# Performance work log

Hardware: AMD Instinct MI355X
Metric: run time of the kernel (lower is better)

Reference implementation:

```python
import jax, jax.numpy as jnp
import numpy as np

B, S, HID = 1, 2048, 1024
NH, NKV, HD = 16, 4, 64
SCALING = 0.125  # attention_multiplier = 1/sqrt(head_dim)
ROPE_THETA = 10000.0
NEG_MIN = jnp.finfo(jnp.float32).min


def rotate_half(x):
    x1, x2 = jnp.split(x, 2, axis=-1)
    return jnp.concatenate([-x2, x1], axis=-1)


def setup_inputs() -> dict:
    key = jax.random.key(0)
    ks = jax.random.split(key, 6)
    hidden_states = jax.random.normal(ks[0], (B, S, HID), dtype=jnp.float32)
    # RoPE tables: [1, 1, S, HD]
    inv_freq = 1.0 / (ROPE_THETA ** (np.arange(0, HD, 2, dtype=np.float32) / HD))
    t = np.arange(S, dtype=np.float32)
    freqs = np.outer(t, inv_freq)                      # [S, HD/2]
    emb = np.concatenate([freqs, freqs], axis=-1)      # [S, HD]
    cos = jnp.asarray(np.cos(emb))[None, None]
    sin = jnp.asarray(np.sin(emb))[None, None]
    attention_mask = jnp.ones((B, S), dtype=bool)
    sc = 0.02
    Wq = jax.random.normal(ks[1], (HID, NH * HD), dtype=jnp.float32) * sc
    Wk = jax.random.normal(ks[2], (HID, NKV * HD), dtype=jnp.float32) * sc
    Wv = jax.random.normal(ks[3], (HID, NKV * HD), dtype=jnp.float32) * sc
    Wo = jax.random.normal(ks[4], (NH * HD, HID), dtype=jnp.float32) * sc
    return {"hidden_states": hidden_states, "cos": cos, "sin": sin,
            "attention_mask": attention_mask, "Wq": Wq, "Wk": Wk, "Wv": Wv, "Wo": Wo}


def reference(hidden_states, cos, sin, attention_mask, Wq, Wk, Wv, Wo):
    b, s, _ = hidden_states.shape
    # projections -> [B, H, S, D]
    q = (hidden_states @ Wq).reshape(b, s, NH, HD).transpose(0, 2, 1, 3)
    k = (hidden_states @ Wk).reshape(b, s, NKV, HD).transpose(0, 2, 1, 3)
    v = (hidden_states @ Wv).reshape(b, s, NKV, HD).transpose(0, 2, 1, 3)
    # RoPE (full head_dim rotation; cos/sin broadcast over batch/heads)
    q = q * cos + rotate_half(q) * sin
    k = k * cos + rotate_half(k) * sin
    # repeat_kv: expand kv heads to match query heads
    n_rep = NH // NKV
    k = jnp.repeat(k, n_rep, axis=1)
    v = jnp.repeat(v, n_rep, axis=1)
    # scores: [B, H, Sq, Sk]
    attn = jnp.einsum('bhqd,bhkd->bhqk', q, k) * SCALING
    mask = attention_mask[:, None, None, :].astype(attn.dtype)  # bool padding mask
    attn = attn + (1.0 - mask) * NEG_MIN
    attn = jax.nn.softmax(attn.astype(jnp.float32), axis=-1).astype(q.dtype)
    out = jnp.einsum('bhqk,bhkd->bhqd', attn, v)
    out = out.transpose(0, 2, 1, 3).reshape(b, s, NH * HD)
    return out @ Wo
```

## Files before the change

kernel.cpp:

```cpp
#include <hip/hip_runtime.h>
#include <stdint.h>

typedef __attribute__((ext_vector_type(8))) short short8;
typedef __attribute__((ext_vector_type(4))) short short4v;
typedef __attribute__((ext_vector_type(4))) float floatx4;
typedef __attribute__((ext_vector_type(16))) float floatx16;
typedef __attribute__((ext_vector_type(2))) unsigned int uint2v;
typedef __attribute__((ext_vector_type(4))) unsigned int uint4v;

#define AS1 __attribute__((address_space(1)))
#define AS3 __attribute__((address_space(3)))

__device__ __forceinline__ void async16(const void* g, void* l) {
  __builtin_amdgcn_global_load_lds((const AS1 unsigned int*)g, (AS3 unsigned int*)l, 16, 0, 0);
}

__device__ __forceinline__ short f2bf(float f) {
  unsigned u = __float_as_uint(f);
  u = (u + 0x7FFF + ((u >> 16) & 1)) >> 16;
  return (short)u;
}

#if __has_builtin(__builtin_amdgcn_cvt_pk_bf16_f32)
typedef __bf16 bf16x2 __attribute__((ext_vector_type(2)));
__device__ __forceinline__ unsigned pack2(float lo, float hi) {
  bf16x2 t = __builtin_amdgcn_cvt_pk_bf16_f32(lo, hi);
  return *(unsigned*)&t;
}
#else
__device__ __forceinline__ unsigned pack2(float lo, float hi) {
  return __builtin_amdgcn_perm(__float_as_uint(hi) + 0x8000u,
                               __float_as_uint(lo) + 0x8000u, 0x07060302u);
}
#endif

__device__ __forceinline__ uint2v permswap32(unsigned a, unsigned b) {
#if __has_builtin(__builtin_amdgcn_permlane32_swap)
  return __builtin_amdgcn_permlane32_swap(a, b, false, false);
#else
  asm volatile("v_permlane32_swap_b32 %0, %1" : "+v"(a), "+v"(b));
  uint2v r; r.x = a; r.y = b; return r;
#endif
}

__device__ __forceinline__ void stage_sw(const short* src, int stride,
                                         short* tile, int cb, int lane) {
  int i = cb + lane;
  int r = i >> 3, j = i & 7;
  async16(src + (size_t)r * stride + ((j ^ (r & 7)) * 8), tile + cb * 8);
}
__device__ __forceinline__ int sw(int row, int c8) {
  return row * 64 + ((c8 ^ (row & 7)) * 8);
}

__global__ void k_prep(const float* __restrict__ X, const float* __restrict__ Wq,
                       const float* __restrict__ Wk, const float* __restrict__ Wv,
                       const float* __restrict__ Wo, short* __restrict__ Xb,
                       short* __restrict__ Wqkvt, short* __restrict__ Wot) {
  int b = blockIdx.x, tid = threadIdx.x;
  if (b < 2048) {
    int i = b * 1024 + tid * 4;
    floatx4 v = *(const floatx4*)(X + i);
    short4v o;
    o.x = f2bf(v.x); o.y = f2bf(v.y); o.z = f2bf(v.z); o.w = f2bf(v.w);
    *(short4v*)(Xb + i) = o;
    return;
  }
  const float* src; short* dst; int N, brel, rowoff;
  if (b < 3072)      { src = Wq; dst = Wqkvt; N = 1024; brel = b - 2048; rowoff = 0; }
  else if (b < 3328) { src = Wk; dst = Wqkvt; N = 256;  brel = b - 3072; rowoff = 1024; }
  else if (b < 3584) { src = Wv; dst = Wqkvt; N = 256;  brel = b - 3328; rowoff = 1280; }
  else               { src = Wo; dst = Wot;   N = 1024; brel = b - 3584; rowoff = 0; }
  __shared__ short t[32][33];
  int nt = N >> 5;
  int n0 = (brel % nt) * 32, k0 = (brel / nt) * 32;
  int tx = tid & 31, ty = tid >> 5;
#pragma unroll
  for (int i = 0; i < 4; i++)
    t[ty + 8 * i][tx] = f2bf(src[(size_t)(k0 + ty + 8 * i) * N + n0 + tx]);
  __syncthreads();
#pragma unroll
  for (int i = 0; i < 4; i++)
    dst[(size_t)(rowoff + n0 + ty + 8 * i) * 1024 + k0 + tx] = t[tx][ty + 8 * i];
}

__global__ __launch_bounds__(256) void k_gemmqkv(const short* __restrict__ A,
                                                 const short* __restrict__ Bt,
                                                 short* __restrict__ Qb,
                                                 short* __restrict__ Kb,
                                                 short* __restrict__ Vtb,
                                                 const float* __restrict__ cosp,
                                                 const float* __restrict__ sinp,
                                                 float qscale) {
  int tid = threadIdx.x;
  int flat = blockIdx.y * 24 + blockIdx.x;
  int swz = (flat & 7) * 96 + (flat >> 3);
  int bx = swz % 24, by = swz / 24;
  int w = tid >> 6, lane = tid & 63, quad = lane >> 4, l16 = lane & 15;
  __shared__ short As[2][4096];
  __shared__ short Bs[2][4096];
  const int K = 1024;
  const short* Ag = A + (size_t)(by * 64) * K;
  const short* Bg = Bt + (size_t)(bx * 64) * K;
  floatx4 acc[4] = {};
#pragma unroll
  for (int t = 0; t < 2; t++) stage_sw(Ag, K, As[0], (w * 2 + t) * 64, lane);
#pragma unroll
  for (int t = 0; t < 2; t++) stage_sw(Bg, K, Bs[0], (w * 2 + t) * 64, lane);
  for (int kt = 0; kt < 16; kt++) {
    __syncthreads();
    int cur = kt & 1, nxt = cur ^ 1;
    if (kt + 1 < 16) {
#pragma unroll
      for (int t = 0; t < 2; t++) stage_sw(Ag + (kt + 1) * 64, K, As[nxt], (w * 2 + t) * 64, lane);
#pragma unroll
      for (int t = 0; t < 2; t++) stage_sw(Bg + (kt + 1) * 64, K, Bs[nxt], (w * 2 + t) * 64, lane);
    }
#pragma unroll
    for (int ks = 0; ks < 2; ks++) {
      short8 af = *(const short8*)&As[cur][sw(w * 16 + l16, ks * 4 + quad)];
#pragma unroll
      for (int j = 0; j < 4; j++) {
        short8 bfr = *(const short8*)&Bs[cur][sw(j * 16 + l16, ks * 4 + quad)];
        acc[j] = __builtin_amdgcn_mfma_f32_16x16x32_bf16(af, bfr, acc[j], 0, 0, 0);
      }
    }
  }
  if (bx < 20) {
    short* dst; float scale;
    if (bx < 16) { dst = Qb + (size_t)bx * 2048 * 64; scale = qscale; }
    else         { dst = Kb + (size_t)(bx - 16) * 2048 * 64; scale = 1.0f; }
#pragma unroll
    for (int r = 0; r < 4; r++) {
      int s = by * 64 + w * 16 + quad * 4 + r;
#pragma unroll
      for (int j = 0; j < 2; j++) {
        int d = j * 16 + l16;
        float c = cosp[s * 64 + d], sn = sinp[s * 64 + d];
        float v0 = acc[j][r], v1 = acc[j + 2][r];
        dst[(size_t)s * 64 + d]      = f2bf((v0 * c - v1 * sn) * scale);
        dst[(size_t)s * 64 + 32 + d] = f2bf((v1 * c + v0 * sn) * scale);
      }
    }
  } else {
    short* dst = Vtb + (size_t)(bx - 20) * 64 * 2048;
#pragma unroll
    for (int j = 0; j < 4; j++) {
      int d = j * 16 + l16;
      short4v pk;
#pragma unroll
      for (int r = 0; r < 4; r++) pk[r] = f2bf(acc[j][r]);
      *(short4v*)&dst[(size_t)d * 2048 + by * 64 + w * 16 + quad * 4] = pk;
    }
  }
}

__global__ __launch_bounds__(256) void k_gemm(const short* __restrict__ A,
                                              const short* __restrict__ Bt,
                                              float* __restrict__ C,
                                              int M, int N, int K) {
  int tid = threadIdx.x;
  int flat = blockIdx.y * 16 + blockIdx.x;
  int swz = (flat & 7) * 64 + (flat >> 3);
  int bx = swz & 15, by = swz >> 4;
  int w = tid >> 6, lane = tid & 63, quad = lane >> 4, l16 = lane & 15;
  __shared__ short As[2][4096];
  __shared__ short Bs[2][4096];
  const short* Ag = A + (size_t)(by * 64) * K;
  const short* Bg = Bt + (size_t)(bx * 64) * K;
  floatx4 acc[4] = {};
  int kiters = K >> 6;
#pragma unroll
  for (int t = 0; t < 2; t++) stage_sw(Ag, K, As[0], (w * 2 + t) * 64, lane);
#pragma unroll
  for (int t = 0; t < 2; t++) stage_sw(Bg, K, Bs[0], (w * 2 + t) * 64, lane);
  for (int kt = 0; kt < kiters; kt++) {
    __syncthreads();
    int cur = kt & 1, nxt = cur ^ 1;
    if (kt + 1 < kiters) {
#pragma unroll
      for (int t = 0; t < 2; t++) stage_sw(Ag + (kt + 1) * 64, K, As[nxt], (w * 2 + t) * 64, lane);
#pragma unroll
      for (int t = 0; t < 2; t++) stage_sw(Bg + (kt + 1) * 64, K, Bs[nxt], (w * 2 + t) * 64, lane);
    }
#pragma unroll
    for (int ks = 0; ks < 2; ks++) {
      short8 af = *(const short8*)&As[cur][sw(w * 16 + l16, ks * 4 + quad)];
#pragma unroll
      for (int j = 0; j < 4; j++) {
        short8 bfr = *(const short8*)&Bs[cur][sw(j * 16 + l16, ks * 4 + quad)];
        acc[j] = __builtin_amdgcn_mfma_f32_16x16x32_bf16(af, bfr, acc[j], 0, 0, 0);
      }
    }
  }
#pragma unroll
  for (int j = 0; j < 4; j++)
#pragma unroll
    for (int r = 0; r < 4; r++) {
      int row = by * 64 + w * 16 + quad * 4 + r;
      int col = bx * 64 + j * 16 + l16;
      __builtin_nontemporal_store(acc[j][r], &C[(size_t)row * N + col]);
    }
}

__global__ __launch_bounds__(256, 4) void k_attn(const short* __restrict__ Qb,
                                                 const short* __restrict__ Kb,
                                                 const short* __restrict__ Vt,
                                                 float* __restrict__ Opart,
                                                 float* __restrict__ lpart) {
  int flat = (blockIdx.z * 16 + blockIdx.y) * 16 + blockIdx.x;
  int swz = (flat & 7) * 128 + (flat >> 3);
  int qt = swz & 15;
  int h = (swz >> 4) & 15;
  int sp = swz >> 8;
  int kvh = h >> 2;
  int tid = threadIdx.x, w = tid >> 6, lane = tid & 63;
  int l32 = lane & 31, hi = lane >> 5;
  __shared__ short Ks[2][4096];
  __shared__ short Vs[2][4096];
  const short* Qg = Qb + ((size_t)h * 2048 + qt * 128 + w * 32) * 64;
  const short* Kg0 = Kb + ((size_t)kvh * 2048 + sp * 512) * 64;
  const short* Vg0 = Vt + (size_t)kvh * 64 * 2048 + sp * 512;
  short8 qf[4];
#pragma unroll
  for (int ks4 = 0; ks4 < 4; ks4++)
    qf[ks4] = *(const short8*)(Qg + l32 * 64 + ks4 * 16 + hi * 8);
#pragma unroll
  for (int t = 0; t < 2; t++) stage_sw(Kg0, 64, Ks[0], (w * 2 + t) * 64, lane);
#pragma unroll
  for (int t = 0; t < 2; t++) stage_sw(Vg0, 2048, Vs[0], (w * 2 + t) * 64, lane);
  short8 vones;
  {
    short one = (short)0x3F80;
#pragma unroll
    for (int j = 0; j < 8; j++) vones[j] = (l32 == 0) ? one : (short)0;
  }
  floatx16 accO[2] = {};
  floatx16 accL = {};
  for (int kt = 0; kt < 8; kt++) {
    __syncthreads();
    if (kt + 1 < 8) {
      int nb = (kt + 1) & 1;
#pragma unroll
      for (int t = 0; t < 2; t++)
        stage_sw(Kg0 + (kt + 1) * 4096, 64, Ks[nb], (w * 2 + t) * 64, lane);
#pragma unroll
      for (int t = 0; t < 2; t++)
        stage_sw(Vg0 + (kt + 1) * 64, 2048, Vs[nb], (w * 2 + t) * 64, lane);
    }
    int cu = kt & 1;
#pragma unroll
    for (int kb = 0; kb < 2; kb++) {
      floatx16 accS = {};
#pragma unroll
      for (int ks4 = 0; ks4 < 4; ks4++) {
        short8 af = *(const short8*)&Ks[cu][sw(kb * 32 + l32, ks4 * 2 + hi)];
        accS = __builtin_amdgcn_mfma_f32_32x32x16_bf16(af, qf[ks4], accS, 0, 0, 0);
      }
#pragma unroll
      for (int c = 0; c < 2; c++) {
        float p0 = __builtin_amdgcn_exp2f(accS[8 * c + 0]);
        float p1 = __builtin_amdgcn_exp2f(accS[8 * c + 1]);
        float p2 = __builtin_amdgcn_exp2f(accS[8 * c + 2]);
        float p3 = __builtin_amdgcn_exp2f(accS[8 * c + 3]);
        float p4 = __builtin_amdgcn_exp2f(accS[8 * c + 4]);
        float p5 = __builtin_amdgcn_exp2f(accS[8 * c + 5]);
        float p6 = __builtin_amdgcn_exp2f(accS[8 * c + 6]);
        float p7 = __builtin_amdgcn_exp2f(accS[8 * c + 7]);
        uint2v r0 = permswap32(pack2(p0, p1), pack2(p4, p5));
        uint2v r1 = permswap32(pack2(p2, p3), pack2(p6, p7));
        uint4v pw; pw.x = r0.x; pw.y = r1.x; pw.z = r0.y; pw.w = r1.y;
        short8 pa = *(short8*)&pw;
        int kstep = kb * 2 + c;
        accL = __builtin_amdgcn_mfma_f32_32x32x16_bf16(pa, vones, accL, 0, 0, 0);
#pragma unroll
        for (int db = 0; db < 2; db++) {
          short8 vf = *(const short8*)&Vs[cu][sw(db * 32 + l32, kstep * 2 + hi)];
          accO[db] = __builtin_amdgcn_mfma_f32_32x32x16_bf16(pa, vf, accO[db], 0, 0, 0);
        }
      }
    }
  }
  if (l32 == 0) {
#pragma unroll
    for (int reg = 0; reg < 16; reg++) {
      int q = (reg & 3) + 8 * (reg >> 2) + 4 * hi;
      __builtin_nontemporal_store(accL[reg],
          &lpart[(size_t)sp * 16 * 2048 + h * 2048 + qt * 128 + w * 32 + q]);
    }
  }
  float* Op = Opart + (size_t)sp * 2048 * 1024;
#pragma unroll
  for (int db = 0; db < 2; db++)
#pragma unroll
    for (int reg = 0; reg < 16; reg++) {
      int q = (reg & 3) + 8 * (reg >> 2) + 4 * hi;
      int srow = qt * 128 + w * 32 + q;
      int col = h * 64 + db * 32 + l32;
      __builtin_nontemporal_store(accO[db][reg], &Op[(size_t)srow * 1024 + col]);
    }
}

__global__ void k_comb(const float* __restrict__ Opart, const float* __restrict__ lpart,
                       short* __restrict__ AOb) {
  int idx = (blockIdx.x * 256 + threadIdx.x) * 4;
  int s = idx >> 10, h = (idx & 1023) >> 6;
  float l = 0.f;
#pragma unroll
  for (int sp = 0; sp < 4; sp++)
    l += __builtin_nontemporal_load(&lpart[sp * 16 * 2048 + h * 2048 + s]);
  float inv = 1.0f / l;
  floatx4 a = __builtin_nontemporal_load((const floatx4*)(Opart + idx));
#pragma unroll
  for (int sp = 1; sp < 4; sp++) {
    floatx4 b = __builtin_nontemporal_load(
        (const floatx4*)(Opart + (size_t)sp * 2048 * 1024 + idx));
    a.x += b.x; a.y += b.y; a.z += b.z; a.w += b.w;
  }
  uint2v pk;
  pk.x = pack2(a.x * inv, a.y * inv);
  pk.y = pack2(a.z * inv, a.w * inv);
  *(uint2v*)&AOb[idx] = pk;
}

extern "C" void kernel_launch(void* const* d_in, const int* in_sizes, int n_in,
                              void* d_out, int out_size, void* d_ws, size_t ws_size,
                              hipStream_t stream) {
  const float* X    = (const float*)d_in[0];
  const float* cosp = (const float*)d_in[1];
  const float* sinp = (const float*)d_in[2];
  const float* Wq = (const float*)d_in[4];
  const float* Wk = (const float*)d_in[5];
  const float* Wv = (const float*)d_in[6];
  const float* Wo = (const float*)d_in[7];
  float* out = (float*)d_out;

  short* Xb    = (short*)d_ws;
  short* Wqkvt = Xb + 2097152;
  short* Wot   = Wqkvt + 1572864;
  short* Qb2   = Wot + 1048576;
  short* Kb2   = Qb2 + 2097152;
  short* Vtb   = Kb2 + 524288;
  short* AOb   = Vtb + 524288;
  float* Opart = (float*)(AOb + 2097152);
  float* lpart = Opart + 4 * 2097152;

  const float QSCALE = 0.125f * 1.44269504088896340736f;

  k_prep<<<4608, 256, 0, stream>>>(X, Wq, Wk, Wv, Wo, Xb, Wqkvt, Wot);
  k_gemmqkv<<<dim3(24, 32), 256, 0, stream>>>(Xb, Wqkvt, Qb2, Kb2, Vtb, cosp, sinp, QSCALE);
  k_attn<<<dim3(16, 16, 4), 256, 0, stream>>>(Qb2, Kb2, Vtb, Opart, lpart);
  k_comb<<<2048, 256, 0, stream>>>(Opart, lpart, AOb);
  k_gemm<<<dim3(16, 32), 256, 0, stream>>>(AOb, Wot, out, 2048, 1024, 1024);
}
```

Before: 138.3 us.

## Process two query groups per wave in attention to reuse K/V fragments

The attention kernel now runs 2 waves per block instead of 4, and each wave handles 64 query rows as two 32-row groups. K and V fragments are loaded from LDS once per key block and reused across both groups, halving LDS reads per MFMA. Each wave also issues twice the staging copies. The cost is more accumulator registers per wave and fewer waves per block, which may lower occupancy and latency hiding.

```diff
diff --git a/kernel.cpp b/kernel.cpp
--- a/kernel.cpp
+++ b/kernel.cpp
@@ -203,7 +203,7 @@
     }
 }
 
-__global__ __launch_bounds__(256, 4) void k_attn(const short* __restrict__ Qb,
+__global__ __launch_bounds__(128, 2) void k_attn(const short* __restrict__ Qb,
                                                  const short* __restrict__ Kb,
                                                  const short* __restrict__ Vt,
                                                  float* __restrict__ Opart,
@@ -218,87 +218,101 @@
   int l32 = lane & 31, hi = lane >> 5;
   __shared__ short Ks[2][4096];
   __shared__ short Vs[2][4096];
-  const short* Qg = Qb + ((size_t)h * 2048 + qt * 128 + w * 32) * 64;
+  const short* Qg = Qb + ((size_t)h * 2048 + qt * 128 + w * 64) * 64;
   const short* Kg0 = Kb + ((size_t)kvh * 2048 + sp * 512) * 64;
   const short* Vg0 = Vt + (size_t)kvh * 64 * 2048 + sp * 512;
-  short8 qf[4];
-#pragma unroll
-  for (int ks4 = 0; ks4 < 4; ks4++)
-    qf[ks4] = *(const short8*)(Qg + l32 * 64 + ks4 * 16 + hi * 8);
-#pragma unroll
-  for (int t = 0; t < 2; t++) stage_sw(Kg0, 64, Ks[0], (w * 2 + t) * 64, lane);
-#pragma unroll
-  for (int t = 0; t < 2; t++) stage_sw(Vg0, 2048, Vs[0], (w * 2 + t) * 64, lane);
+  short8 qf[2][4];
+#pragma unroll
+  for (int g = 0; g < 2; g++)
+#pragma unroll
+    for (int ks4 = 0; ks4 < 4; ks4++)
+      qf[g][ks4] = *(const short8*)(Qg + (g * 32 + l32) * 64 + ks4 * 16 + hi * 8);
+#pragma unroll
+  for (int t = 0; t < 4; t++) stage_sw(Kg0, 64, Ks[0], (w * 4 + t) * 64, lane);
+#pragma unroll
+  for (int t = 0; t < 4; t++) stage_sw(Vg0, 2048, Vs[0], (w * 4 + t) * 64, lane);
   short8 vones;
   {
     short one = (short)0x3F80;
 #pragma unroll
     for (int j = 0; j < 8; j++) vones[j] = (l32 == 0) ? one : (short)0;
   }
-  floatx16 accO[2] = {};
-  floatx16 accL = {};
+  floatx16 accO[2][2] = {};
+  floatx16 accL[2] = {};
   for (int kt = 0; kt < 8; kt++) {
     __syncthreads();
     if (kt + 1 < 8) {
       int nb = (kt + 1) & 1;
 #pragma unroll
-      for (int t = 0; t < 2; t++)
-        stage_sw(Kg0 + (kt + 1) * 4096, 64, Ks[nb], (w * 2 + t) * 64, lane);
-#pragma unroll
-      for (int t = 0; t < 2; t++)
-        stage_sw(Vg0 + (kt + 1) * 64, 2048, Vs[nb], (w * 2 + t) * 64, lane);
+      for (int t = 0; t < 4; t++)
+        stage_sw(Kg0 + (kt + 1) * 4096, 64, Ks[nb], (w * 4 + t) * 64, lane);
+#pragma unroll
+      for (int t = 0; t < 4; t++)
+        stage_sw(Vg0 + (kt + 1) * 64, 2048, Vs[nb], (w * 4 + t) * 64, lane);
     }
     int cu = kt & 1;
 #pragma unroll
     for (int kb = 0; kb < 2; kb++) {
-      floatx16 accS = {};
-#pragma unroll
-      for (int ks4 = 0; ks4 < 4; ks4++) {
-        short8 af = *(const short8*)&Ks[cu][sw(kb * 32 + l32, ks4 * 2 + hi)];
-        accS = __builtin_amdgcn_mfma_f32_32x32x16_bf16(af, qf[ks4], accS, 0, 0, 0);
-      }
-#pragma unroll
-      for (int c = 0; c < 2; c++) {
-        float p0 = __builtin_amdgcn_exp2f(accS[8 * c + 0]);
-        float p1 = __builtin_amdgcn_exp2f(accS[8 * c + 1]);
-        float p2 = __builtin_amdgcn_exp2f(accS[8 * c + 2]);
-        float p3 = __builtin_amdgcn_exp2f(accS[8 * c + 3]);
-        float p4 = __builtin_amdgcn_exp2f(accS[8 * c + 4]);
-        float p5 = __builtin_amdgcn_exp2f(accS[8 * c + 5]);
-        float p6 = __builtin_amdgcn_exp2f(accS[8 * c + 6]);
-        float p7 = __builtin_amdgcn_exp2f(accS[8 * c + 7]);
-        uint2v r0 = permswap32(pack2(p0, p1), pack2(p4, p5));
-        uint2v r1 = permswap32(pack2(p2, p3), pack2(p6, p7));
-        uint4v pw; pw.x = r0.x; pw.y = r1.x; pw.z = r0.y; pw.w = r1.y;
-        short8 pa = *(short8*)&pw;
-        int kstep = kb * 2 + c;
-        accL = __builtin_amdgcn_mfma_f32_32x32x16_bf16(pa, vones, accL, 0, 0, 0);
-#pragma unroll
-        for (int db = 0; db < 2; db++) {
-          short8 vf = *(const short8*)&Vs[cu][sw(db * 32 + l32, kstep * 2 + hi)];
-          accO[db] = __builtin_amdgcn_mfma_f32_32x32x16_bf16(pa, vf, accO[db], 0, 0, 0);
+      short8 af[4];
+#pragma unroll
+      for (int ks4 = 0; ks4 < 4; ks4++)
+        af[ks4] = *(const short8*)&Ks[cu][sw(kb * 32 + l32, ks4 * 2 + hi)];
+      short8 vf[2][2];
+#pragma unroll
+      for (int c = 0; c < 2; c++)
+#pragma unroll
+        for (int db = 0; db < 2; db++)
+          vf[c][db] = *(const short8*)&Vs[cu][sw(db * 32 + l32, (kb * 2 + c) * 2 + hi)];
+#pragma unroll
+      for (int g = 0; g < 2; g++) {
+        floatx16 accS = {};
+#pragma unroll
+        for (int ks4 = 0; ks4 < 4; ks4++)
+          accS = __builtin_amdgcn_mfma_f32_32x32x16_bf16(af[ks4], qf[g][ks4], accS, 0, 0, 0);
+#pragma unroll
+        for (int c = 0; c < 2; c++) {
+          float p0 = __builtin_amdgcn_exp2f(accS[8 * c + 0]);
+          float p1 = __builtin_amdgcn_exp2f(accS[8 * c + 1]);
+          float p2 = __builtin_amdgcn_exp2f(accS[8 * c + 2]);
+          float p3 = __builtin_amdgcn_exp2f(accS[8 * c + 3]);
+          float p4 = __builtin_amdgcn_exp2f(accS[8 * c + 4]);
+          float p5 = __builtin_amdgcn_exp2f(accS[8 * c + 5]);
+          float p6 = __builtin_amdgcn_exp2f(accS[8 * c + 6]);
+          float p7 = __builtin_amdgcn_exp2f(accS[8 * c + 7]);
+          uint2v r0 = permswap32(pack2(p0, p1), pack2(p4, p5));
+          uint2v r1 = permswap32(pack2(p2, p3), pack2(p6, p7));
+          uint4v pw; pw.x = r0.x; pw.y = r1.x; pw.z = r0.y; pw.w = r1.y;
+          short8 pa = *(short8*)&pw;
+          accL[g] = __builtin_amdgcn_mfma_f32_32x32x16_bf16(pa, vones, accL[g], 0, 0, 0);
+#pragma unroll
+          for (int db = 0; db < 2; db++)
+            accO[g][db] = __builtin_amdgcn_mfma_f32_32x32x16_bf16(pa, vf[c][db], accO[g][db], 0, 0, 0);
         }
       }
     }
   }
   if (l32 == 0) {
 #pragma unroll
-    for (int reg = 0; reg < 16; reg++) {
-      int q = (reg & 3) + 8 * (reg >> 2) + 4 * hi;
-      __builtin_nontemporal_store(accL[reg],
-          &lpart[(size_t)sp * 16 * 2048 + h * 2048 + qt * 128 + w * 32 + q]);
-    }
+    for (int g = 0; g < 2; g++)
+#pragma unroll
+      for (int reg = 0; reg < 16; reg++) {
+        int q = (reg & 3) + 8 * (reg >> 2) + 4 * hi;
+        __builtin_nontemporal_store(accL[g][reg],
+            &lpart[(size_t)sp * 16 * 2048 + h * 2048 + qt * 128 + w * 64 + g * 32 + q]);
+      }
   }
   float* Op = Opart + (size_t)sp * 2048 * 1024;
 #pragma unroll
-  for (int db = 0; db < 2; db++)
-#pragma unroll
-    for (int reg = 0; reg < 16; reg++) {
-      int q = (reg & 3) + 8 * (reg >> 2) + 4 * hi;
-      int srow = qt * 128 + w * 32 + q;
-      int col = h * 64 + db * 32 + l32;
-      __builtin_nontemporal_store(accO[db][reg], &Op[(size_t)srow * 1024 + col]);
-    }
+  for (int g = 0; g < 2; g++)
+#pragma unroll
+    for (int db = 0; db < 2; db++)
+#pragma unroll
+      for (int reg = 0; reg < 16; reg++) {
+        int q = (reg & 3) + 8 * (reg >> 2) + 4 * hi;
+        int srow = qt * 128 + w * 64 + g * 32 + q;
+        int col = h * 64 + db * 32 + l32;
+        __builtin_nontemporal_store(accO[g][db][reg], &Op[(size_t)srow * 1024 + col]);
+      }
 }
 
 __global__ void k_comb(const float* __restrict__ Opart, const float* __restrict__ lpart,
@@ -349,7 +363,7 @@
 
   k_prep<<<4608, 256, 0, stream>>>(X, Wq, Wk, Wv, Wo, Xb, Wqkvt, Wot);
   k_gemmqkv<<<dim3(24, 32), 256, 0, stream>>>(Xb, Wqkvt, Qb2, Kb2, Vtb, cosp, sinp, QSCALE);
-  k_attn<<<dim3(16, 16, 4), 256, 0, stream>>>(Qb2, Kb2, Vtb, Opart, lpart);
+  k_attn<<<dim3(16, 16, 4), 128, 0, stream>>>(Qb2, Kb2, Vtb, Opart, lpart);
   k_comb<<<2048, 256, 0, stream>>>(Opart, lpart, AOb);
   k_gemm<<<dim3(16, 32), 256, 0, stream>>>(AOb, Wot, out, 2048, 1024, 1024);
 }
```

Measured after the change: 139.6 us. Within noise of the previous version (+0.9%).

## Drop split-K attention and fuse normalization into attention with triple buffering

Applied to the files above, without the earlier changes.

Attention blocks now iterate over the whole key sequence instead of one quarter, normalizing the output in-kernel and writing bf16 directly. This eliminates the fp32 partial output buffers and the separate combine kernel. K/V staging moves to a three-stage ring with explicit vmcnt waits and raw barriers. The trade-off is a quarter as many blocks with four times the serial work each, lowering parallelism per CU.

```diff
diff --git a/kernel.cpp b/kernel.cpp
--- a/kernel.cpp
+++ b/kernel.cpp
@@ -42,6 +42,8 @@
   uint2v r; r.x = a; r.y = b; return r;
 #endif
 }
+
+#define WAITVM(N) asm volatile("s_waitcnt vmcnt(" #N ")" ::: "memory")
 
 __device__ __forceinline__ void stage_sw(const short* src, int stride,
                                          short* tile, int cb, int lane) {
@@ -203,32 +205,33 @@
     }
 }
 
-__global__ __launch_bounds__(256, 4) void k_attn(const short* __restrict__ Qb,
-                                                 const short* __restrict__ Kb,
-                                                 const short* __restrict__ Vt,
-                                                 float* __restrict__ Opart,
-                                                 float* __restrict__ lpart) {
-  int flat = (blockIdx.z * 16 + blockIdx.y) * 16 + blockIdx.x;
-  int swz = (flat & 7) * 128 + (flat >> 3);
+__global__ __launch_bounds__(256) void k_attn(const short* __restrict__ Qb,
+                                              const short* __restrict__ Kb,
+                                              const short* __restrict__ Vt,
+                                              short* __restrict__ AOb) {
+  int flat = blockIdx.y * 16 + blockIdx.x;
+  int swz = (flat & 7) * 32 + (flat >> 3);
   int qt = swz & 15;
-  int h = (swz >> 4) & 15;
-  int sp = swz >> 8;
+  int h = swz >> 4;
   int kvh = h >> 2;
   int tid = threadIdx.x, w = tid >> 6, lane = tid & 63;
   int l32 = lane & 31, hi = lane >> 5;
-  __shared__ short Ks[2][4096];
-  __shared__ short Vs[2][4096];
+  __shared__ short Ks[3][4096];
+  __shared__ short Vs[3][4096];
   const short* Qg = Qb + ((size_t)h * 2048 + qt * 128 + w * 32) * 64;
-  const short* Kg0 = Kb + ((size_t)kvh * 2048 + sp * 512) * 64;
-  const short* Vg0 = Vt + (size_t)kvh * 64 * 2048 + sp * 512;
+  const short* Kg0 = Kb + (size_t)kvh * 2048 * 64;
+  const short* Vg0 = Vt + (size_t)kvh * 64 * 2048;
   short8 qf[4];
 #pragma unroll
   for (int ks4 = 0; ks4 < 4; ks4++)
     qf[ks4] = *(const short8*)(Qg + l32 * 64 + ks4 * 16 + hi * 8);
 #pragma unroll
-  for (int t = 0; t < 2; t++) stage_sw(Kg0, 64, Ks[0], (w * 2 + t) * 64, lane);
-#pragma unroll
-  for (int t = 0; t < 2; t++) stage_sw(Vg0, 2048, Vs[0], (w * 2 + t) * 64, lane);
+  for (int p = 0; p < 2; p++) {
+#pragma unroll
+    for (int t = 0; t < 2; t++) stage_sw(Kg0 + p * 4096, 64, Ks[p], (w * 2 + t) * 64, lane);
+#pragma unroll
+    for (int t = 0; t < 2; t++) stage_sw(Vg0 + p * 64, 2048, Vs[p], (w * 2 + t) * 64, lane);
+  }
   short8 vones;
   {
     short one = (short)0x3F80;
@@ -237,24 +240,25 @@
   }
   floatx16 accO[2] = {};
   floatx16 accL = {};
-  for (int kt = 0; kt < 8; kt++) {
-    __syncthreads();
-    if (kt + 1 < 8) {
-      int nb = (kt + 1) & 1;
+  int cur = 0;
+  for (int kt = 0; kt < 32; kt++) {
+    if (kt < 31) WAITVM(4); else WAITVM(0);
+    __builtin_amdgcn_s_barrier();
+    if (kt + 2 < 32) {
+      int stg = cur ? cur - 1 : 2;
 #pragma unroll
       for (int t = 0; t < 2; t++)
-        stage_sw(Kg0 + (kt + 1) * 4096, 64, Ks[nb], (w * 2 + t) * 64, lane);
+        stage_sw(Kg0 + (kt + 2) * 4096, 64, Ks[stg], (w * 2 + t) * 64, lane);
 #pragma unroll
       for (int t = 0; t < 2; t++)
-        stage_sw(Vg0 + (kt + 1) * 64, 2048, Vs[nb], (w * 2 + t) * 64, lane);
-    }
-    int cu = kt & 1;
+        stage_sw(Vg0 + (kt + 2) * 64, 2048, Vs[stg], (w * 2 + t) * 64, lane);
+    }
 #pragma unroll
     for (int kb = 0; kb < 2; kb++) {
       floatx16 accS = {};
 #pragma unroll
       for (int ks4 = 0; ks4 < 4; ks4++) {
-        short8 af = *(const short8*)&Ks[cu][sw(kb * 32 + l32, ks4 * 2 + hi)];
+        short8 af = *(const short8*)&Ks[cur][sw(kb * 32 + l32, ks4 * 2 + hi)];
         accS = __builtin_amdgcn_mfma_f32_32x32x16_bf16(af, qf[ks4], accS, 0, 0, 0);
       }
 #pragma unroll
@@ -275,52 +279,25 @@
         accL = __builtin_amdgcn_mfma_f32_32x32x16_bf16(pa, vones, accL, 0, 0, 0);
 #pragma unroll
         for (int db = 0; db < 2; db++) {
-          short8 vf = *(const short8*)&Vs[cu][sw(db * 32 + l32, kstep * 2 + hi)];
+          short8 vf = *(const short8*)&Vs[cur][sw(db * 32 + l32, kstep * 2 + hi)];
           accO[db] = __builtin_amdgcn_mfma_f32_32x32x16_bf16(pa, vf, accO[db], 0, 0, 0);
         }
       }
     }
-  }
-  if (l32 == 0) {
-#pragma unroll
-    for (int reg = 0; reg < 16; reg++) {
-      int q = (reg & 3) + 8 * (reg >> 2) + 4 * hi;
-      __builtin_nontemporal_store(accL[reg],
-          &lpart[(size_t)sp * 16 * 2048 + h * 2048 + qt * 128 + w * 32 + q]);
-    }
-  }
-  float* Op = Opart + (size_t)sp * 2048 * 1024;
-#pragma unroll
-  for (int db = 0; db < 2; db++)
-#pragma unroll
-    for (int reg = 0; reg < 16; reg++) {
-      int q = (reg & 3) + 8 * (reg >> 2) + 4 * hi;
-      int srow = qt * 128 + w * 32 + q;
+    cur = (cur == 2) ? 0 : cur + 1;
+  }
+#pragma unroll
+  for (int reg = 0; reg < 16; reg++) {
+    float l = __shfl(accL[reg], lane & 32, 64);
+    float inv = 1.0f / l;
+    int q = (reg & 3) + 8 * (reg >> 2) + 4 * hi;
+    int srow = qt * 128 + w * 32 + q;
+#pragma unroll
+    for (int db = 0; db < 2; db++) {
       int col = h * 64 + db * 32 + l32;
-      __builtin_nontemporal_store(accO[db][reg], &Op[(size_t)srow * 1024 + col]);
-    }
-}
-
-__global__ void k_comb(const float* __restrict__ Opart, const float* __restrict__ lpart,
-                       short* __restrict__ AOb) {
-  int idx = (blockIdx.x * 256 + threadIdx.x) * 4;
-  int s = idx >> 10, h = (idx & 1023) >> 6;
-  float l = 0.f;
-#pragma unroll
-  for (int sp = 0; sp < 4; sp++)
-    l += __builtin_nontemporal_load(&lpart[sp * 16 * 2048 + h * 2048 + s]);
-  float inv = 1.0f / l;
-  floatx4 a = __builtin_nontemporal_load((const floatx4*)(Opart + idx));
-#pragma unroll
-  for (int sp = 1; sp < 4; sp++) {
-    floatx4 b = __builtin_nontemporal_load(
-        (const floatx4*)(Opart + (size_t)sp * 2048 * 1024 + idx));
-    a.x += b.x; a.y += b.y; a.z += b.z; a.w += b.w;
-  }
-  uint2v pk;
-  pk.x = pack2(a.x * inv, a.y * inv);
-  pk.y = pack2(a.z * inv, a.w * inv);
-  *(uint2v*)&AOb[idx] = pk;
+      AOb[(size_t)srow * 1024 + col] = f2bf(accO[db][reg] * inv);
+    }
+  }
 }
 
 extern "C" void kernel_launch(void* const* d_in, const int* in_sizes, int n_in,
@@ -342,14 +319,11 @@
   short* Kb2   = Qb2 + 2097152;
   short* Vtb   = Kb2 + 524288;
   short* AOb   = Vtb + 524288;
-  float* Opart = (float*)(AOb + 2097152);
-  float* lpart = Opart + 4 * 2097152;
 
   const float QSCALE = 0.125f * 1.44269504088896340736f;
 
   k_prep<<<4608, 256, 0, stream>>>(X, Wq, Wk, Wv, Wo, Xb, Wqkvt, Wot);
   k_gemmqkv<<<dim3(24, 32), 256, 0, stream>>>(Xb, Wqkvt, Qb2, Kb2, Vtb, cosp, sinp, QSCALE);
-  k_attn<<<dim3(16, 16, 4), 256, 0, stream>>>(Qb2, Kb2, Vtb, Opart, lpart);
-  k_comb<<<2048, 256, 0, stream>>>(Opart, lpart, AOb);
+  k_attn<<<dim3(16, 16), 256, 0, stream>>>(Qb2, Kb2, Vtb, AOb);
   k_gemm<<<dim3(16, 32), 256, 0, stream>>>(AOb, Wot, out, 2048, 1024, 1024);
 }
```

Measured after the change: 151.4 us. 1.09x slower.
